# Kernel optimization log

Hardware: AMD Instinct MI355X
Metric: run time of the kernel (lower is better)

The kernel has to match this reference:

```python
import jax, jax.numpy as jnp
import numpy as np
from jax import lax

# Faithful JAX translation of ConvAttention (enc=True, mask=False), the core
# kernel-headroom op of Conv_Transformer. Key observation: the per-(s,t)-pair
# conv2 over concat(Q[...,s], K[...,t]) is linear, so it decomposes exactly as
# conv(Q_s, W_q) + conv(K_t, W_k) + bias, where W_q/W_k are the first/second
# half of conv2's input channels. This reproduces the same math without
# materializing the [b, 2c, h, w, s, t] tensor or looping over time.

B, C, H, W, S = 4, 64, 64, 64, 20
K_SIZE = 3


def _conv_same(x, w):
    # x: [N, Cin, H, W], w: [Cout, Cin, kh, kw]
    return lax.conv_general_dilated(
        x, w, window_strides=(1, 1), padding='SAME',
        dimension_numbers=('NCHW', 'OIHW', 'NCHW'))


def setup_inputs() -> dict:
    key = jax.random.key(0)
    k1, k2, k3, k4, k5 = jax.random.split(key, 5)
    x = jax.random.normal(k1, (B, C, H, W, S), dtype=jnp.float32)
    w1 = jax.random.normal(k2, (3 * C, C, 1, 1), dtype=jnp.float32) * 0.05
    b1 = jax.random.normal(k3, (3 * C,), dtype=jnp.float32) * 0.05
    w2 = jax.random.normal(k4, (1, 2 * C, K_SIZE, K_SIZE), dtype=jnp.float32) * 0.05
    b2 = jax.random.normal(k5, (1,), dtype=jnp.float32) * 0.05
    return {'x': x, 'w1': w1, 'b1': b1, 'w2': w2, 'b2': b2}


def reference(x, w1, b1, w2, b2):
    b, c, h, w, s = x.shape
    # conv1 (1x1) per timestep -> QKV: [b, 3c, h, w, s]
    qkv = jnp.einsum('bchws,oc->bohws', x, w1[:, :, 0, 0]) \
        + b1[None, :, None, None, None]
    Q, K, V = jnp.split(qkv, 3, axis=1)  # each [b, c, h, w, s]

    # Decompose conv2 over concatenated channels.
    Wq, Wk = w2[:, :c], w2[:, c:]  # each [1, c, kh, kw]

    def per_time_conv(t5, wgt):
        # t5: [b, c, h, w, s] -> scores [b, h, w, s]
        flat = jnp.moveaxis(t5, -1, 1).reshape(b * s, c, h, w)
        out = _conv_same(flat, wgt)  # [b*s, 1, h, w]
        return out.reshape(b, s, h, w).transpose(0, 2, 3, 1)

    A = per_time_conv(Q, Wq)  # [b, h, w, s]  (query index)
    Bk = per_time_conv(K, Wk)  # [b, h, w, t]  (key index)

    # score[b,h,w,t,s] = conv2(concat(Q_s, K_t)) ; softmax over t (keys)
    scores = A[:, :, :, None, :] + Bk[:, :, :, :, None] + b2[0]
    attn = jax.nn.softmax(scores, axis=-2)  # [b, h, w, t, s]

    # V_out[b,c,h,w,s] = sum_t attn[...,t,s] * V[...,t]
    V_out = jnp.einsum('bhwts,bchwt->bchws', attn, V)
    return V_out
```

## Files before the change

kernel.cpp:

```cpp
#include <hip/hip_runtime.h>
#include <math.h>

#define Bb 4
#define Cc 64
#define Hh 64
#define Ww 64
#define Ss 20

constexpr int XC = Hh * Ww * Ss;
constexpr int XH = Ww * Ss;
constexpr int XW = Ss;
constexpr int XB = Cc * XC;


__global__ void ct_fold_weights(const float* __restrict__ w1,
                                const float* __restrict__ b1,
                                const float* __restrict__ w2,
                                float* __restrict__ ws) {
    int tid = threadIdx.x;
    if (tid < 576) {
        int tap = tid >> 6, cp = tid & 63;
        float acc = 0.f;
        #pragma unroll 8
        for (int c = 0; c < 64; ++c)
            acc += w2[(64 + c) * 9 + tap] * w1[(64 + c) * 64 + cp];
        ws[tid] = acc;
    } else if (tid < 585) {
        int tap = tid - 576;
        float acc = 0.f;
        for (int c = 0; c < 64; ++c)
            acc += w2[(64 + c) * 9 + tap] * b1[64 + c];
        ws[576 + tap] = acc;
    }
}

__global__ __launch_bounds__(320, 5) void ct_fused(
        const float* __restrict__ x,
        const float* __restrict__ w1,
        const float* __restrict__ b1,
        const float* __restrict__ ws,
        float* __restrict__ out) {
    __shared__ float weff[576];
    __shared__ float btL[9];
    __shared__ float w1t[64 * 65];
    __shared__ float bkp[4][16][20];
    __shared__ float psm[16][20];
    __shared__ float xsh[16][65];
    int tid = threadIdx.x;

    for (int i = tid; i < 576; i += 320) weff[i] = ws[i];
    if (tid < 9) btL[tid] = ws[576 + tid];
    #pragma unroll
    for (int k = 0; k < 13; ++k) {
        int j = tid + k * 320;
        if (j < 4096) {
            int r = j >> 6, q = j & 63;
            w1t[q * 65 + r] = w1[8192 + j];
        }
    }

    int g = (blockIdx.x & 7) * 128 + (blockIdx.x >> 3);
    int wq = g & 3;
    int h  = (g >> 2) & 63;
    int b  = g >> 8;

    int w16 = (tid / 5) & 15, t4 = tid % 5, cg = tid / 80;
    int w = wq * 16 + w16;

    float vmask[9];
    int off[9];
    #pragma unroll
    for (int dh = 0; dh < 3; ++dh) {
        int hh = h + dh - 1;
        float hv = (hh >= 0 && hh < Hh) ? 1.f : 0.f;
        int hcl = hh < 0 ? 0 : (hh > Hh - 1 ? Hh - 1 : hh);
        #pragma unroll
        for (int dw = 0; dw < 3; ++dw) {
            int wc = w + dw - 1;
            float wvd = (wc >= 0 && wc < Ww) ? 1.f : 0.f;
            int wcl = wc < 0 ? 0 : (wc > Ww - 1 ? Ww - 1 : wc);
            vmask[dh * 3 + dw] = hv * wvd;
            off[dh * 3 + dw] = hcl * XH + wcl * XW;
        }
    }
    __syncthreads();

    float4 acc = make_float4(0.f, 0.f, 0.f, 0.f);
    const float* xb = x + b * XB + cg * 16 * XC + t4 * 4;
    #pragma unroll 2
    for (int i = 0; i < 16; ++i) {
        const float* xc = xb + i * XC;
        #pragma unroll
        for (int tap = 0; tap < 9; ++tap) {
            float wv = weff[tap * 64 + cg * 16 + i] * vmask[tap];
            const float4 xv = *reinterpret_cast<const float4*>(xc + off[tap]);
            acc.x = fmaf(wv, xv.x, acc.x);
            acc.y = fmaf(wv, xv.y, acc.y);
            acc.z = fmaf(wv, xv.z, acc.z);
            acc.w = fmaf(wv, xv.w, acc.w);
        }
    }
    *reinterpret_cast<float4*>(&bkp[cg][w16][t4 * 4]) = acc;
    __syncthreads();

    {
        int sw = tid / 20, t = tid % 20;
        float v = bkp[0][sw][t] + bkp[1][sw][t] + bkp[2][sw][t] + bkp[3][sw][t];
        int wsite = wq * 16 + sw;
        float bs = 0.f;
        #pragma unroll
        for (int dh = 0; dh < 3; ++dh) {
            int hh = h + dh - 1;
            if (hh < 0 || hh >= Hh) continue;
            #pragma unroll
            for (int dw = 0; dw < 3; ++dw) {
                int wc = wsite + dw - 1;
                if (wc < 0 || wc >= Ww) continue;
                bs += btL[dh * 3 + dw];
            }
        }
        psm[sw][t] = v + bs;
    }
    __syncthreads();

    if (tid < 16) {
        float p[20];
        #pragma unroll
        for (int i = 0; i < 20; ++i) p[i] = psm[tid][i];
        float m = p[0];
        #pragma unroll
        for (int i = 1; i < 20; ++i) m = fmaxf(m, p[i]);
        float ssum = 0.f;
        #pragma unroll
        for (int i = 0; i < 20; ++i) { p[i] = __expf(p[i] - m); ssum += p[i]; }
        float inv = 1.f / ssum;
        #pragma unroll
        for (int i = 0; i < 20; ++i) psm[tid][i] = p[i] * inv;
    }
    __syncthreads();

    int si = tid & 15, cq = tid >> 4;
    int wsite = wq * 16 + si;
    if (cq < 16) {
        #pragma unroll
        for (int k = 0; k < 4; ++k) {
            int c = cq * 4 + k;
            const float* xp = x + (b * 64 + c) * XC + h * XH + wsite * 20;
            float xbv = 0.f;
            #pragma unroll
            for (int i = 0; i < 5; ++i) {
                float4 xv = reinterpret_cast<const float4*>(xp)[i];
                xbv = fmaf(psm[si][4 * i],     xv.x, xbv);
                xbv = fmaf(psm[si][4 * i + 1], xv.y, xbv);
                xbv = fmaf(psm[si][4 * i + 2], xv.z, xbv);
                xbv = fmaf(psm[si][4 * i + 3], xv.w, xbv);
            }
            xsh[si][c] = xbv;
        }
    }
    __syncthreads();

    if (cq < 16) {
        #pragma unroll
        for (int k = 0; k < 4; ++k) {
            int c = cq * 4 + k;
            float R = b1[128 + c];
            #pragma unroll 8
            for (int cp = 0; cp < 64; ++cp)
                R = fmaf(w1t[cp * 65 + c], xsh[si][cp], R);
            float* op = out + (b * 64 + c) * XC + h * XH + wsite * 20;
            float4 rv = make_float4(R, R, R, R);
            #pragma unroll
            for (int s4 = 0; s4 < 5; ++s4)
                reinterpret_cast<float4*>(op)[s4] = rv;
        }
    }
}

extern "C" void kernel_launch(void* const* d_in, const int* in_sizes, int n_in,
                              void* d_out, int out_size, void* d_ws, size_t ws_size,
                              hipStream_t stream) {
    const float* x  = (const float*)d_in[0];
    const float* w1 = (const float*)d_in[1];
    const float* b1 = (const float*)d_in[2];
    const float* w2 = (const float*)d_in[3];
    float* ws  = (float*)d_ws;
    float* out = (float*)d_out;

    ct_fold_weights<<<1, 640, 0, stream>>>(w1, b1, w2, ws);
    ct_fused<<<1024, 320, 0, stream>>>(x, w1, b1, ws, out);
}
```

Before: 84.12 us.

## Split fused kernel into conv+softmax and attention-output kernels via workspace

Breaks the single fused kernel into two. The first computes the key-conv scores and softmax over 32 w-sites per block and writes probabilities to a global workspace. The second kernel reads them back and does the V reduction and 1x1 projection over 8 sites per block with 2048 blocks. The aim is to raise occupancy and parallelism in the attention phase, which no longer has to share a large block with the conv. The cost is an extra kernel launch, a global round trip for the probabilities, and reloading w1 into shared memory in many more blocks.

```diff
diff --git a/kernel.cpp b/kernel.cpp
--- a/kernel.cpp
+++ b/kernel.cpp
@@ -11,6 +11,8 @@
 constexpr int XH = Ww * Ss;
 constexpr int XW = Ss;
 constexpr int XB = Cc * XC;
+constexpr int NSITE = Bb * Hh * Ww;
+constexpr int PSMF  = NSITE * Ss;
 
 
 __global__ void ct_fold_weights(const float* __restrict__ w1,
@@ -34,38 +36,27 @@
     }
 }
 
-__global__ __launch_bounds__(320, 5) void ct_fused(
+__global__ __launch_bounds__(640) void ct_conv_sm(
         const float* __restrict__ x,
-        const float* __restrict__ w1,
-        const float* __restrict__ b1,
         const float* __restrict__ ws,
-        float* __restrict__ out) {
+        float* __restrict__ psm) {
     __shared__ float weff[576];
     __shared__ float btL[9];
-    __shared__ float w1t[64 * 65];
-    __shared__ float bkp[4][16][20];
-    __shared__ float psm[16][20];
-    __shared__ float xsh[16][65];
+    __shared__ float bkp[4][32][20];
+    __shared__ float psmL[32][20];
     int tid = threadIdx.x;
 
-    for (int i = tid; i < 576; i += 320) weff[i] = ws[i];
+    for (int i = tid; i < 576; i += 640) weff[i] = ws[i];
     if (tid < 9) btL[tid] = ws[576 + tid];
-    #pragma unroll
-    for (int k = 0; k < 13; ++k) {
-        int j = tid + k * 320;
-        if (j < 4096) {
-            int r = j >> 6, q = j & 63;
-            w1t[q * 65 + r] = w1[8192 + j];
-        }
-    }
-
-    int g = (blockIdx.x & 7) * 128 + (blockIdx.x >> 3);
-    int wq = g & 3;
-    int h  = (g >> 2) & 63;
-    int b  = g >> 8;
-
-    int w16 = (tid / 5) & 15, t4 = tid % 5, cg = tid / 80;
-    int w = wq * 16 + w16;
+
+    int g = (blockIdx.x & 7) * 64 + (blockIdx.x >> 3);
+    int wh = g & 1;
+    int h  = (g >> 1) & 63;
+    int b  = g >> 7;
+
+    int cg = tid / 160, r = tid % 160;
+    int w16 = r / 5, t4 = r % 5;
+    int w = wh * 32 + w16;
 
     float vmask[9];
     int off[9];
@@ -88,11 +79,11 @@
     float4 acc = make_float4(0.f, 0.f, 0.f, 0.f);
     const float* xb = x + b * XB + cg * 16 * XC + t4 * 4;
     #pragma unroll 2
-    for (int i = 0; i < 16; ++i) {
-        const float* xc = xb + i * XC;
+    for (int c = 0; c < 16; ++c) {
+        const float* xc = xb + c * XC;
         #pragma unroll
         for (int tap = 0; tap < 9; ++tap) {
-            float wv = weff[tap * 64 + cg * 16 + i] * vmask[tap];
+            float wv = weff[tap * 64 + cg * 16 + c] * vmask[tap];
             const float4 xv = *reinterpret_cast<const float4*>(xc + off[tap]);
             acc.x = fmaf(wv, xv.x, acc.x);
             acc.y = fmaf(wv, xv.y, acc.y);
@@ -106,7 +97,7 @@
     {
         int sw = tid / 20, t = tid % 20;
         float v = bkp[0][sw][t] + bkp[1][sw][t] + bkp[2][sw][t] + bkp[3][sw][t];
-        int wsite = wq * 16 + sw;
+        int wsit = wh * 32 + sw;
         float bs = 0.f;
         #pragma unroll
         for (int dh = 0; dh < 3; ++dh) {
@@ -114,19 +105,19 @@
             if (hh < 0 || hh >= Hh) continue;
             #pragma unroll
             for (int dw = 0; dw < 3; ++dw) {
-                int wc = wsite + dw - 1;
+                int wc = wsit + dw - 1;
                 if (wc < 0 || wc >= Ww) continue;
                 bs += btL[dh * 3 + dw];
             }
         }
-        psm[sw][t] = v + bs;
-    }
-    __syncthreads();
-
-    if (tid < 16) {
+        psmL[sw][t] = v + bs;
+    }
+    __syncthreads();
+
+    if (tid < 32) {
         float p[20];
         #pragma unroll
-        for (int i = 0; i < 20; ++i) p[i] = psm[tid][i];
+        for (int i = 0; i < 20; ++i) p[i] = psmL[tid][i];
         float m = p[0];
         #pragma unroll
         for (int i = 1; i < 20; ++i) m = fmaxf(m, p[i]);
@@ -135,45 +126,74 @@
         for (int i = 0; i < 20; ++i) { p[i] = __expf(p[i] - m); ssum += p[i]; }
         float inv = 1.f / ssum;
         #pragma unroll
-        for (int i = 0; i < 20; ++i) psm[tid][i] = p[i] * inv;
-    }
-    __syncthreads();
-
-    int si = tid & 15, cq = tid >> 4;
-    int wsite = wq * 16 + si;
-    if (cq < 16) {
-        #pragma unroll
-        for (int k = 0; k < 4; ++k) {
-            int c = cq * 4 + k;
-            const float* xp = x + (b * 64 + c) * XC + h * XH + wsite * 20;
-            float xbv = 0.f;
-            #pragma unroll
-            for (int i = 0; i < 5; ++i) {
-                float4 xv = reinterpret_cast<const float4*>(xp)[i];
-                xbv = fmaf(psm[si][4 * i],     xv.x, xbv);
-                xbv = fmaf(psm[si][4 * i + 1], xv.y, xbv);
-                xbv = fmaf(psm[si][4 * i + 2], xv.z, xbv);
-                xbv = fmaf(psm[si][4 * i + 3], xv.w, xbv);
-            }
-            xsh[si][c] = xbv;
-        }
-    }
-    __syncthreads();
-
-    if (cq < 16) {
-        #pragma unroll
-        for (int k = 0; k < 4; ++k) {
-            int c = cq * 4 + k;
-            float R = b1[128 + c];
-            #pragma unroll 8
-            for (int cp = 0; cp < 64; ++cp)
-                R = fmaf(w1t[cp * 65 + c], xsh[si][cp], R);
-            float* op = out + (b * 64 + c) * XC + h * XH + wsite * 20;
-            float4 rv = make_float4(R, R, R, R);
-            #pragma unroll
-            for (int s4 = 0; s4 < 5; ++s4)
-                reinterpret_cast<float4*>(op)[s4] = rv;
-        }
+        for (int i = 0; i < 20; ++i) psmL[tid][i] = p[i] * inv;
+    }
+    __syncthreads();
+
+    {
+        int sw = tid / 20, t = tid % 20;
+        int site = b * 4096 + h * 64 + wh * 32 + sw;
+        psm[site * 20 + t] = psmL[sw][t];
+    }
+}
+
+__global__ __launch_bounds__(256) void ct_attn_lite(
+        const float* __restrict__ x,
+        const float* __restrict__ w1,
+        const float* __restrict__ b1,
+        const float* __restrict__ psm,
+        float* __restrict__ out) {
+    __shared__ float w1t[64 * 65];
+    __shared__ float psmL[8][20];
+    __shared__ float xsh[8][65];
+    int tid = threadIdx.x;
+    #pragma unroll
+    for (int k = 0; k < 16; ++k) {
+        int j = tid + k * 256;
+        int r = j >> 6, q = j & 63;
+        w1t[q * 65 + r] = w1[8192 + j];
+    }
+
+    int site0 = blockIdx.x * 8;
+    if (tid < 160) {
+        int si = tid / 20, i = tid % 20;
+        psmL[si][i] = psm[(site0 + si) * 20 + i];
+    }
+    __syncthreads();
+
+    int si = tid & 7, cg = tid >> 3;
+    int site = site0 + si;
+    int b = site >> 12, hw = site & 4095;
+
+    #pragma unroll
+    for (int k = 0; k < 2; ++k) {
+        int c = cg * 2 + k;
+        const float* xp = x + (b * 64 + c) * XC + hw * 20;
+        float xbv = 0.f;
+        #pragma unroll
+        for (int i = 0; i < 5; ++i) {
+            float4 xv = reinterpret_cast<const float4*>(xp)[i];
+            xbv = fmaf(psmL[si][4 * i],     xv.x, xbv);
+            xbv = fmaf(psmL[si][4 * i + 1], xv.y, xbv);
+            xbv = fmaf(psmL[si][4 * i + 2], xv.z, xbv);
+            xbv = fmaf(psmL[si][4 * i + 3], xv.w, xbv);
+        }
+        xsh[si][c] = xbv;
+    }
+    __syncthreads();
+
+    #pragma unroll
+    for (int k = 0; k < 2; ++k) {
+        int c = cg * 2 + k;
+        float R = b1[128 + c];
+        #pragma unroll 8
+        for (int cp = 0; cp < 64; ++cp)
+            R = fmaf(w1t[cp * 65 + c], xsh[si][cp], R);
+        float* op = out + (b * 64 + c) * XC + hw * 20;
+        float4 rv = make_float4(R, R, R, R);
+        #pragma unroll
+        for (int s4 = 0; s4 < 5; ++s4)
+            reinterpret_cast<float4*>(op)[s4] = rv;
     }
 }
 
@@ -185,8 +205,10 @@
     const float* b1 = (const float*)d_in[2];
     const float* w2 = (const float*)d_in[3];
     float* ws  = (float*)d_ws;
+    float* psm = ws + 640;
     float* out = (float*)d_out;
 
     ct_fold_weights<<<1, 640, 0, stream>>>(w1, b1, w2, ws);
-    ct_fused<<<1024, 320, 0, stream>>>(x, w1, b1, ws, out);
-}
+    ct_conv_sm<<<512, 640, 0, stream>>>(x, ws, psm);
+    ct_attn_lite<<<2048, 256, 0, stream>>>(x, w1, b1, psm, out);
+}
```

Result: faster. 74.28 us (-11.7%).
